# Optimization experiments

Hardware: AMD Instinct MI355X
Metric: run time of the kernel (lower is better)

The kernel has to match this reference:

```python
import jax, jax.numpy as jnp
import numpy as np

D_ATTN = 2048
D_STATE = 64
SHIFT_FRAC = 0.5
LN_EPS = 1e-5


def setup_inputs() -> dict:
    key = jax.random.key(0)
    ks = jax.random.split(key, 8)
    B, T = 8, 2048
    s_attn = 1.0 / np.sqrt(D_ATTN)
    s_state = 1.0 / np.sqrt(D_STATE)
    x = jax.random.normal(ks[0], (B, T, D_ATTN), jnp.float32)
    W_key = jax.random.normal(ks[1], (D_STATE, D_ATTN), jnp.float32) * s_attn
    W_value = jax.random.normal(ks[2], (D_STATE, D_ATTN), jnp.float32) * s_attn
    W_output = jax.random.normal(ks[3], (D_ATTN, D_STATE), jnp.float32) * s_state
    W_shift = jax.random.normal(ks[4], (D_ATTN, D_ATTN), jnp.float32) * s_attn
    gate = jnp.ones((D_ATTN,), jnp.float32)
    # negative decay log so w = exp(time_decay) in (e^-1, 1): stable over T=2048 steps
    time_decay = -jax.random.uniform(ks[5], (D_STATE,), jnp.float32, 0.05, 1.0)
    time_first = jax.random.normal(ks[6], (D_STATE,), jnp.float32) * 0.1
    ln_gamma = jnp.ones((D_ATTN,), jnp.float32)
    ln_beta = jnp.zeros((D_ATTN,), jnp.float32)
    return dict(x=x, W_key=W_key, W_value=W_value, W_output=W_output,
                W_shift=W_shift, gate=gate, time_decay=time_decay,
                time_first=time_first, ln_gamma=ln_gamma, ln_beta=ln_beta)


def reference(x, W_key, W_value, W_output, W_shift, gate, time_decay,
              time_first, ln_gamma, ln_beta):
    B, T, D = x.shape
    # token shift: cat([x[:, s:], x[:, :-s]], dim=1) == roll(x, -s, axis=1)
    shift_len = max(1, int(T * SHIFT_FRAC))
    x_cat = jnp.roll(x, -shift_len, axis=1)
    g = jax.nn.sigmoid(gate)
    x_shift = jnp.einsum('btd,ed->bte', x_cat, W_shift) * g + x * (1.0 - g)
    # LayerNorm over last dim
    mu = jnp.mean(x_shift, axis=-1, keepdims=True)
    var = jnp.var(x_shift, axis=-1, keepdims=True)
    x_norm = (x_shift - mu) * jax.lax.rsqrt(var + LN_EPS) * ln_gamma + ln_beta
    k = jnp.einsum('btd,sd->bts', x_norm, W_key)    # (B,T,Ds)
    v = jnp.einsum('btd,sd->bts', x_norm, W_value)  # (B,T,Ds)
    w = jnp.exp(time_decay)                          # (Ds,)
    u = jnp.exp(time_first)                          # (Ds,)
    wkv = jnp.exp(-u * jax.nn.sigmoid(k)) * v        # (B,T,Ds)
    # linear recurrence: state_t = w * state_{t-1} + wkv_t
    def step(state, wkv_t):
        state = state * w + wkv_t
        return state, state
    init = jnp.zeros((B, k.shape[-1]), x.dtype)
    last_state, states = jax.lax.scan(step, init, jnp.swapaxes(wkv, 0, 1))
    states = jnp.swapaxes(states, 0, 1)              # (B,T,Ds)
    # per-step output projection == single batched GEMM over stacked states
    output = jnp.einsum('bts,ds->btd', states, W_output)  # (B,T,D)
    # dropout in eval mode is identity; last_state is detached in original
    return output, jax.lax.stop_gradient(last_state)
```

## Files before the change

### kernel.cpp

```cpp
#include <hip/hip_runtime.h>
#include <stdint.h>

constexpr int kD  = 2048;
constexpr int kDS = 64;
constexpr int kNT = 2048;
constexpr int kM  = 8 * kNT;
constexpr int kOutElems = kM * kD;

typedef __attribute__((ext_vector_type(8))) short short8;
typedef __attribute__((ext_vector_type(8))) unsigned short bfu8;
typedef __attribute__((ext_vector_type(4))) float f32x4;

__device__ __forceinline__ unsigned short f2bf(float f) {
  unsigned int u = __float_as_uint(f);
  return (unsigned short)((u + 0x7FFFu + ((u >> 16) & 1u)) >> 16);
}
__device__ __forceinline__ float bf2f(unsigned short b) {
  return __uint_as_float(((unsigned int)b) << 16);
}

__device__ __forceinline__ void gload16(const void* g, void* l) {
  __builtin_amdgcn_global_load_lds((__attribute__((address_space(1))) void*)g,
                                   (__attribute__((address_space(3))) void*)l,
                                   16, 0, 0);
}

__global__ void k_cvt(const float* __restrict__ src, unsigned short* __restrict__ dst, int n8) {
  int i8 = blockIdx.x * 256 + threadIdx.x;
  if (i8 >= n8) return;
  const f32x4* s = (const f32x4*)(src + (size_t)i8 * 8);
  f32x4 v0 = s[0], v1 = s[1];
  bfu8 o;
  o[0] = f2bf(v0[0]); o[1] = f2bf(v0[1]); o[2] = f2bf(v0[2]); o[3] = f2bf(v0[3]);
  o[4] = f2bf(v1[0]); o[5] = f2bf(v1[1]); o[6] = f2bf(v1[2]); o[7] = f2bf(v1[3]);
  *(bfu8*)(dst + (size_t)i8 * 8) = o;
}

__global__ void k_cvt_kv(const float* __restrict__ wk, const float* __restrict__ wv,
                         unsigned short* __restrict__ dst) {
  int i8 = blockIdx.x * 256 + threadIdx.x;
  int r = i8 >> 8;
  int dcol = (i8 & 255) << 3;
  int s = r >> 1;
  const float* src = (r & 1) ? wv : wk;
  const f32x4* p = (const f32x4*)(src + (size_t)s * kD + dcol);
  f32x4 v0 = p[0], v1 = p[1];
  bfu8 o;
  o[0] = f2bf(v0[0]); o[1] = f2bf(v0[1]); o[2] = f2bf(v0[2]); o[3] = f2bf(v0[3]);
  o[4] = f2bf(v1[0]); o[5] = f2bf(v1[1]); o[6] = f2bf(v1[2]); o[7] = f2bf(v1[3]);
  *(bfu8*)(dst + (size_t)i8 * 8) = o;
}

#define MM(x,y,z) __builtin_amdgcn_mfma_f32_16x16x32_bf16(x,y,z,0,0,0)
#define BAR __builtin_amdgcn_s_barrier()
#define WAITV_(N) asm volatile("s_waitcnt vmcnt(" #N ")" ::: "memory")
#define WAITV(N) WAITV_(N)
#define WAITL asm volatile("s_waitcnt lgkmcnt(0)")
#define NOWV (void)0

#define STAGEA_TO(BUF,H,Q,KT) gload16(aS + (size_t)(((H)*64+(Q)*128)*2048) + (KT), \
                                      smem + (BUF)*32768 + ((H)*64+(Q)*128)*64 + ldsAst)
#define STAGEB_TO(BUF,H,Q,KT) gload16(bS + (size_t)(((H)*32+(Q)*128)*2048) + (KT), \
                                      smem + (BUF)*32768 + 16384 + (H)*2048 + (Q)*8192 + ldsBst)

#define RDA(CUR,H,MF,KS) (*(const short8*)(smem + (CUR)*32768 + ardb + (H)*4096 + (MF)*1024 + colrd##KS))
#define RDB(CUR,H,NF,KS) (*(const short8*)(smem + (CUR)*32768 + 16384 + brdb + (H)*2048 + (NF)*1024 + colrd##KS))

#define RD_A(CUR,H) \
  a[0][0]=RDA(CUR,H,0,0); a[0][1]=RDA(CUR,H,0,1); \
  a[1][0]=RDA(CUR,H,1,0); a[1][1]=RDA(CUR,H,1,1); \
  a[2][0]=RDA(CUR,H,2,0); a[2][1]=RDA(CUR,H,2,1); \
  a[3][0]=RDA(CUR,H,3,0); a[3][1]=RDA(CUR,H,3,1)
#define RD_B(CUR,H,BV) \
  BV[0][0]=RDB(CUR,H,0,0); BV[0][1]=RDB(CUR,H,0,1); \
  BV[1][0]=RDB(CUR,H,1,0); BV[1][1]=RDB(CUR,H,1,1)

#define MF16(MH, B, NB) \
  __builtin_amdgcn_s_setprio(1); \
  acc[(MH)*4+0][(NB)+0] = MM(a[0][0], B[0][0], acc[(MH)*4+0][(NB)+0]); \
  acc[(MH)*4+0][(NB)+1] = MM(a[0][0], B[1][0], acc[(MH)*4+0][(NB)+1]); \
  acc[(MH)*4+1][(NB)+0] = MM(a[1][0], B[0][0], acc[(MH)*4+1][(NB)+0]); \
  acc[(MH)*4+1][(NB)+1] = MM(a[1][0], B[1][0], acc[(MH)*4+1][(NB)+1]); \
  acc[(MH)*4+2][(NB)+0] = MM(a[2][0], B[0][0], acc[(MH)*4+2][(NB)+0]); \
  acc[(MH)*4+2][(NB)+1] = MM(a[2][0], B[1][0], acc[(MH)*4+2][(NB)+1]); \
  acc[(MH)*4+3][(NB)+0] = MM(a[3][0], B[0][0], acc[(MH)*4+3][(NB)+0]); \
  acc[(MH)*4+3][(NB)+1] = MM(a[3][0], B[1][0], acc[(MH)*4+3][(NB)+1]); \
  acc[(MH)*4+0][(NB)+0] = MM(a[0][1], B[0][1], acc[(MH)*4+0][(NB)+0]); \
  acc[(MH)*4+0][(NB)+1] = MM(a[0][1], B[1][1], acc[(MH)*4+0][(NB)+1]); \
  acc[(MH)*4+1][(NB)+0] = MM(a[1][1], B[0][1], acc[(MH)*4+1][(NB)+0]); \
  acc[(MH)*4+1][(NB)+1] = MM(a[1][1], B[1][1], acc[(MH)*4+1][(NB)+1]); \
  acc[(MH)*4+2][(NB)+0] = MM(a[2][1], B[0][1], acc[(MH)*4+2][(NB)+0]); \
  acc[(MH)*4+2][(NB)+1] = MM(a[2][1], B[1][1], acc[(MH)*4+2][(NB)+1]); \
  acc[(MH)*4+3][(NB)+0] = MM(a[3][1], B[0][1], acc[(MH)*4+3][(NB)+0]); \
  acc[(MH)*4+3][(NB)+1] = MM(a[3][1], B[1][1], acc[(MH)*4+3][(NB)+1]); \
  __builtin_amdgcn_s_setprio(0)

#define PH0(CUR, S, KA1, WV) \
  BAR; WAITL; MF16(0, b0, 0); \
  RD_B(CUR,1,b1); \
  if (S) { STAGEA_TO((CUR)^1, 1, 0, KA1); STAGEA_TO((CUR)^1, 1, 1, KA1); } \
  WV

#define PH1(CUR, S, KT2, WV) \
  BAR; WAITL; MF16(0, b1, 2); \
  RD_A(CUR,1); \
  if (S) { STAGEA_TO(CUR, 0, 0, KT2); STAGEA_TO(CUR, 0, 1, KT2); } \
  WV

#define PH2(CUR, S, KT2, WV) \
  BAR; WAITL; MF16(1, b0, 0); \
  if (S) { STAGEB_TO(CUR, 0, 0, KT2); STAGEB_TO(CUR, 0, 1, KT2); } \
  WV

#define PH3(CUR, RDN, S, KT2, WV) \
  BAR; WAITL; MF16(1, b1, 2); \
  if (RDN) { RD_A((CUR)^1,0); RD_B((CUR)^1,0,b0); } \
  if (S) { STAGEB_TO(CUR, 1, 0, KT2); STAGEB_TO(CUR, 1, 1, KT2); } \
  WV

__global__ __launch_bounds__(512, 2)
void k_gemm_shift8(const unsigned short* __restrict__ A,
                   const unsigned short* __restrict__ Bw,
                   const float* __restrict__ gate,
                   unsigned short* __restrict__ out) {
  __shared__ __align__(16) unsigned char smem_raw[131072];
  unsigned short* smem = (unsigned short*)smem_raw;

  const int tid = threadIdx.x;
  const int lane = tid & 63;
  const int w = tid >> 6;
  const int wr = w >> 2, wc = w & 3;
  const int lr = lane & 15, lq = lane >> 4;
  const int bid = blockIdx.x;
  const int nblk = bid & 7, mblk = bid >> 3;
  const int m0 = mblk * 256, n0 = nblk * 256;

  const int r0 = tid >> 3;
  const int colel = ((tid & 7) * 8) ^ (((tid >> 3) & 7) << 3);
  const unsigned short* aS = A + (size_t)((m0 ^ 1024) + r0) * 2048 + colel;
  const unsigned short* bS = Bw + (size_t)(n0 + ((tid >> 8) << 6) + (r0 & 31)) * 2048 + colel;
  const int ldsAst = tid * 8;
  const int ldsBst = ((tid >> 8) << 12) + (tid & 255) * 8;

  const int ardb = (wr * 128 + lr) * 64;
  const int brdb = (wc * 64 + lr) * 64;
  const int colrd0 = (lq * 8) ^ ((lr & 7) << 3);
  const int colrd1 = (32 + lq * 8) ^ ((lr & 7) << 3);

  short8 a[4][2], b0[2][2], b1[2][2];
  f32x4 acc[8][4] = {};

  STAGEA_TO(0,0,0,0); STAGEA_TO(0,0,1,0);
  STAGEB_TO(0,0,0,0); STAGEB_TO(0,0,1,0);
  STAGEB_TO(0,1,0,0); STAGEB_TO(0,1,1,0);
  STAGEA_TO(0,1,0,0); STAGEA_TO(0,1,1,0);
  STAGEA_TO(1,0,0,64); STAGEA_TO(1,0,1,64);
  STAGEB_TO(1,0,0,64); STAGEB_TO(1,0,1,64);
  STAGEB_TO(1,1,0,64); STAGEB_TO(1,1,1,64);
  WAITV(6); BAR;
  RD_A(0,0); RD_B(0,0,b0);

  int ka1 = 64, kt2 = 128;
  for (int j = 0; j < 15; ++j) {
    PH0(0, 1, ka1, WAITV(8)); PH1(0, 1, kt2, WAITV(8));
    PH2(0, 1, kt2, WAITV(8)); PH3(0, 1, 1, kt2, WAITV(8));
    ka1 += 64; kt2 += 64;
    PH0(1, 1, ka1, WAITV(8)); PH1(1, 1, kt2, WAITV(8));
    PH2(1, 1, kt2, WAITV(8)); PH3(1, 1, 1, kt2, WAITV(8));
    ka1 += 64; kt2 += 64;
  }
  PH0(0, 1, 1984, WAITV(8)); PH1(0, 0, 0, NOWV);
  PH2(0, 0, 0, WAITV(4));    PH3(0, 1, 0, 0, WAITV(2));
  PH0(1, 0, 0, WAITV(0));    PH1(1, 0, 0, NOWV);
  PH2(1, 0, 0, NOWV);        PH3(1, 0, 0, 0, NOWV);

  float* cbuf = (float*)smem_raw;
#pragma unroll
  for (int q = 0; q < 4; ++q) {
    __syncthreads();
    if (wr == (q >> 1)) {
#pragma unroll
      for (int mm = 0; mm < 4; ++mm) {
#pragma unroll
        for (int nf = 0; nf < 4; ++nf) {
#pragma unroll
          for (int i = 0; i < 4; ++i) {
            int rl = mm * 16 + lq * 4 + i;
            int cl = wc * 64 + nf * 16 + lr;
            cbuf[rl * 260 + cl] = acc[(q & 1) * 4 + mm][nf][i];
          }
        }
      }
    }
    __syncthreads();
#pragma unroll
    for (int it = 0; it < 4; ++it) {
      int idx = tid + it * 512;
      int rl = idx >> 5, cb = (idx & 31) * 8;
      int gr = m0 + q * 64 + rl, gc = n0 + cb;
      f32x4 c0 = *(const f32x4*)&cbuf[rl * 260 + cb];
      f32x4 c1 = *(const f32x4*)&cbuf[rl * 260 + cb + 4];
      f32x4 g0 = *(const f32x4*)&gate[gc];
      f32x4 g1 = *(const f32x4*)&gate[gc + 4];
      bfu8 xv = *(const bfu8*)(A + (size_t)gr * 2048 + gc);
      bfu8 o;
#pragma unroll
      for (int jj = 0; jj < 4; ++jj) {
        float g = 1.f / (1.f + __expf(-g0[jj]));
        o[jj] = f2bf(c0[jj] * g + bf2f(xv[jj]) * (1.f - g));
        float h = 1.f / (1.f + __expf(-g1[jj]));
        o[jj + 4] = f2bf(c1[jj] * h + bf2f(xv[jj + 4]) * (1.f - h));
      }
      *(bfu8*)(out + (size_t)gr * 2048 + gc) = o;
    }
  }
}

__launch_bounds__(256)
__global__ void k_ln(const unsigned short* __restrict__ xs, const float* __restrict__ gamma,
                     const float* __restrict__ beta, unsigned short* __restrict__ xn) {
  int m = blockIdx.x;
  int tid = threadIdx.x;
  bfu8 v = *(const bfu8*)(xs + (size_t)m * kD + tid * 8);
  float f[8];
#pragma unroll
  for (int j = 0; j < 8; ++j) f[j] = bf2f(v[j]);
  float s = 0.f, q = 0.f;
#pragma unroll
  for (int j = 0; j < 8; ++j) { s += f[j]; q += f[j] * f[j]; }
#pragma unroll
  for (int d = 1; d < 64; d <<= 1) { s += __shfl_xor(s, d); q += __shfl_xor(q, d); }
  __shared__ float ss[4], qq[4];
  if ((tid & 63) == 0) { ss[tid >> 6] = s; qq[tid >> 6] = q; }
  __syncthreads();
  s = ss[0] + ss[1] + ss[2] + ss[3];
  q = qq[0] + qq[1] + qq[2] + qq[3];
  float mean = s * (1.f / kD);
  float var = q * (1.f / kD) - mean * mean;
  float rstd = rsqrtf(var + 1e-5f);
  int d0 = tid * 8;
  bfu8 o;
#pragma unroll
  for (int j = 0; j < 8; ++j) {
    float g = gamma[d0 + j], b = beta[d0 + j];
    o[j] = f2bf((f[j] - mean) * rstd * g + b);
  }
  *(bfu8*)(xn + (size_t)m * kD + d0) = o;
}

__launch_bounds__(256, 2)
__global__ void k_gemm_kv(const unsigned short* __restrict__ A,
                          const unsigned short* __restrict__ Bw,
                          const float* __restrict__ tfirst,
                          float* __restrict__ wkv) {
  __shared__ __align__(16) unsigned short As[32 * 32];
  __shared__ __align__(16) unsigned short Bs[128 * 32];
  const int tid = threadIdx.x;
  const int lane = tid & 63;
  const int wcv = tid >> 6;
  const int m0 = blockIdx.x * 32;
  const int lr = lane & 15, lk = (lane >> 4) << 3;
  const int c1 = tid, c2 = tid + 256;

  const unsigned short* ga = A + (size_t)(m0 + (tid >> 2)) * kD + ((tid & 3) << 3);
  const unsigned short* gb0 = Bw + (size_t)(c1 >> 2) * kD + ((c1 & 3) << 3);
  const unsigned short* gb1 = Bw + (size_t)(c2 >> 2) * kD + ((c2 & 3) << 3);
  unsigned short* la = As + tid * 8;
  unsigned short* lb0 = Bs + c1 * 8;
  unsigned short* lb1 = Bs + c2 * 8;

  f32x4 acc[2][2] = {};

  for (int kt = 0; kt < kD; kt += 32) {
    __syncthreads();
    if (tid < 128) gload16(ga + kt, la);
    gload16(gb0 + kt, lb0);
    gload16(gb1 + kt, lb1);
    __syncthreads();
    short8 af[2], bf[2];
#pragma unroll
    for (int mf = 0; mf < 2; ++mf)
      af[mf] = *(const short8*)&As[(mf * 16 + lr) * 32 + lk];
#pragma unroll
    for (int nf = 0; nf < 2; ++nf)
      bf[nf] = *(const short8*)&Bs[(wcv * 32 + nf * 16 + lr) * 32 + lk];
#pragma unroll
    for (int mf = 0; mf < 2; ++mf)
#pragma unroll
      for (int nf = 0; nf < 2; ++nf)
        acc[mf][nf] = __builtin_amdgcn_mfma_f32_16x16x32_bf16(af[mf], bf[nf], acc[mf][nf], 0, 0, 0);
  }

  const int fq = lane >> 4, fr = lane & 15;
#pragma unroll
  for (int mf = 0; mf < 2; ++mf) {
#pragma unroll
    for (int nf = 0; nf < 2; ++nf) {
      int c = wcv * 32 + nf * 16 + fr;
#pragma unroll
      for (int i = 0; i < 4; ++i) {
        int r = m0 + mf * 16 + fq * 4 + i;
        float val = acc[mf][nf][i];
        float other = __shfl_xor(val, 1);
        if (!(c & 1)) {
          int s = c >> 1;
          float sk = 1.f / (1.f + expf(-val));
          float u = expf(tfirst[s]);
          wkv[(size_t)r * kDS + s] = expf(-u * sk) * other;
        }
      }
    }
  }
}

__global__ void k_scan(const float* __restrict__ wkv, const float* __restrict__ tdec,
                       unsigned short* __restrict__ states, float* __restrict__ last_state) {
  int chunk = blockIdx.x;
  int b = blockIdx.y;
  int s = threadIdx.x;
  float w = expf(tdec[s]);
  int t1 = chunk * 64;
  int warm = t1 < 256 ? t1 : 256;
  const float* base = wkv + (size_t)b * kNT * kDS + s;
  unsigned short* sbase = states + (size_t)b * kNT * kDS + s;
  float st = 0.f;
#pragma unroll 4
  for (int t = t1 - warm; t < t1; ++t) st = fmaf(st, w, base[(size_t)t * kDS]);
#pragma unroll 4
  for (int t = t1; t < t1 + 64; ++t) {
    st = fmaf(st, w, base[(size_t)t * kDS]);
    sbase[(size_t)t * kDS] = f2bf(st);
  }
  if (chunk == 31) last_state[b * kDS + s] = st;
}

__launch_bounds__(256, 3)
__global__ void k_out_gemm(const unsigned short* __restrict__ states,
                           const unsigned short* __restrict__ Wo,
                           float* __restrict__ out) {
  __shared__ __align__(16) unsigned char sraw[33792];
  unsigned short* As = (unsigned short*)sraw;
  unsigned short* Bs = As + 8192;
  float* cbuf = (float*)sraw;
  const int tid = threadIdx.x;
  const int lane = tid & 63;
  const int w = tid >> 6;
  const int wr = w >> 1, wc = w & 1;
  const int lr = lane & 15, lq = lane >> 4;
  const int n0 = blockIdx.x * 128;
  const int m0 = blockIdx.y * 128;

  const int sr0 = tid >> 3;
  const int scol = ((tid & 7) * 8) ^ (((tid >> 3) & 7) << 3);
#pragma unroll
  for (int rd = 0; rd < 4; ++rd) {
    gload16(states + (size_t)(m0 + sr0 + rd * 32) * 64 + scol, As + tid * 8 + rd * 2048);
    gload16(Wo + (size_t)(n0 + sr0 + rd * 32) * 64 + scol, Bs + tid * 8 + rd * 2048);
  }
  __syncthreads();

  short8 a[4][2], b[4][2];
#pragma unroll
  for (int mf = 0; mf < 4; ++mf) {
#pragma unroll
    for (int ks = 0; ks < 2; ++ks) {
      int col = (ks * 32 + lq * 8) ^ ((lr & 7) << 3);
      a[mf][ks] = *(const short8*)&As[(wr * 64 + mf * 16 + lr) * 64 + col];
      b[mf][ks] = *(const short8*)&Bs[(wc * 64 + mf * 16 + lr) * 64 + col];
    }
  }
  f32x4 acc[4][4] = {};
#pragma unroll
  for (int mf = 0; mf < 4; ++mf)
#pragma unroll
    for (int nf = 0; nf < 4; ++nf) {
      acc[mf][nf] = __builtin_amdgcn_mfma_f32_16x16x32_bf16(a[mf][0], b[nf][0], acc[mf][nf], 0, 0, 0);
      acc[mf][nf] = __builtin_amdgcn_mfma_f32_16x16x32_bf16(a[mf][1], b[nf][1], acc[mf][nf], 0, 0, 0);
    }

#pragma unroll
  for (int q = 0; q < 2; ++q) {
    __syncthreads();
    if (wr == q) {
#pragma unroll
      for (int mf = 0; mf < 4; ++mf)
#pragma unroll
        for (int nf = 0; nf < 4; ++nf)
#pragma unroll
          for (int i = 0; i < 4; ++i) {
            int rl = mf * 16 + lq * 4 + i;
            int cl = wc * 64 + nf * 16 + lr;
            cbuf[rl * 132 + cl] = acc[mf][nf][i];
          }
    }
    __syncthreads();
#pragma unroll
    for (int it = 0; it < 8; ++it) {
      int idx = tid + it * 256;
      int rl = idx >> 5, cb = (idx & 31) * 4;
      *(f32x4*)&out[(size_t)(m0 + q * 64 + rl) * kD + n0 + cb] = *(const f32x4*)&cbuf[rl * 132 + cb];
    }
  }
}

extern "C" void kernel_launch(void* const* d_in, const int* in_sizes, int n_in,
                              void* d_out, int out_size, void* d_ws, size_t ws_size,
                              hipStream_t stream) {
  const float* x    = (const float*)d_in[0];
  const float* Wk   = (const float*)d_in[1];
  const float* Wv   = (const float*)d_in[2];
  const float* Wo   = (const float*)d_in[3];
  const float* Wsh  = (const float*)d_in[4];
  const float* gate = (const float*)d_in[5];
  const float* tdec = (const float*)d_in[6];
  const float* tfir = (const float*)d_in[7];
  const float* lng  = (const float*)d_in[8];
  const float* lnb  = (const float*)d_in[9];
  float* out = (float*)d_out;
  char* ws = (char*)d_ws;

  unsigned short* xbf   = (unsigned short*)(ws);
  unsigned short* wshbf = (unsigned short*)(ws + 67108864);
  unsigned short* wkvbf = (unsigned short*)(ws + 75497472);
  float* wkvf           = (float*)(ws + 76021760);
  unsigned short* stbf  = (unsigned short*)(ws + 80216064);
  unsigned short* wobf  = (unsigned short*)(ws + 82313216);

  k_cvt<<<16384, 256, 0, stream>>>(x, xbf, 4194304);
  k_cvt<<<2048, 256, 0, stream>>>(Wsh, wshbf, 524288);
  k_cvt<<<64, 256, 0, stream>>>(Wo, wobf, 16384);
  k_cvt_kv<<<128, 256, 0, stream>>>(Wk, Wv, wkvbf);

  k_gemm_shift8<<<512, 512, 0, stream>>>(xbf, wshbf, gate, (unsigned short*)out);
  k_ln<<<16384, 256, 0, stream>>>((const unsigned short*)out, lng, lnb, xbf);
  k_gemm_kv<<<512, 256, 0, stream>>>(xbf, wkvbf, tfir, wkvf);
  k_scan<<<dim3(32, 8), 64, 0, stream>>>(wkvf, tdec, stbf, out + kOutElems);
  k_out_gemm<<<dim3(16, 128), 256, 0, stream>>>(stbf, wobf, out);
}
```

Baseline: 289.1 us.

## Fold LayerNorm affine into K/V weights and apply row stats in GEMM epilogue

Replaces the LayerNorm kernel that wrote a normalized bf16 activation with a stats-only kernel that emits per-row mean and rstd. Gamma is folded into the bf16 K/V weights, and per-column sums of gamma*W and beta*W are precomputed. The K/V GEMM now reads the un-normalized shift output directly and applies mean/rstd correction in its epilogue. This removes a full write of the 64MB-class normalized tensor, but the correction k = rstd*(acc - mean*sum) can lose precision through cancellation in bf16-accumulated products.

```diff
diff --git a/kernel.cpp b/kernel.cpp
--- a/kernel.cpp
+++ b/kernel.cpp
@@ -36,19 +36,36 @@
   *(bfu8*)(dst + (size_t)i8 * 8) = o;
 }
 
-__global__ void k_cvt_kv(const float* __restrict__ wk, const float* __restrict__ wv,
-                         unsigned short* __restrict__ dst) {
-  int i8 = blockIdx.x * 256 + threadIdx.x;
-  int r = i8 >> 8;
-  int dcol = (i8 & 255) << 3;
-  int s = r >> 1;
-  const float* src = (r & 1) ? wv : wk;
-  const f32x4* p = (const f32x4*)(src + (size_t)s * kD + dcol);
+__launch_bounds__(256)
+__global__ void k_cvt_kv_g(const float* __restrict__ wk, const float* __restrict__ wv,
+                           const float* __restrict__ gamma, const float* __restrict__ beta,
+                           unsigned short* __restrict__ dst, float2* __restrict__ cgb) {
+  int b = blockIdx.x;
+  int tid = threadIdx.x;
+  int s = b >> 1;
+  const float* src = (b & 1) ? wv : wk;
+  int d0 = tid * 8;
+  const f32x4* p = (const f32x4*)(src + (size_t)s * kD + d0);
   f32x4 v0 = p[0], v1 = p[1];
+  f32x4 g0 = *(const f32x4*)&gamma[d0], g1 = *(const f32x4*)&gamma[d0 + 4];
+  f32x4 b0 = *(const f32x4*)&beta[d0],  b1 = *(const f32x4*)&beta[d0 + 4];
   bfu8 o;
-  o[0] = f2bf(v0[0]); o[1] = f2bf(v0[1]); o[2] = f2bf(v0[2]); o[3] = f2bf(v0[3]);
-  o[4] = f2bf(v1[0]); o[5] = f2bf(v1[1]); o[6] = f2bf(v1[2]); o[7] = f2bf(v1[3]);
-  *(bfu8*)(dst + (size_t)i8 * 8) = o;
+  float sg = 0.f, sb = 0.f;
+#pragma unroll
+  for (int j = 0; j < 4; ++j) {
+    float gw0 = g0[j] * v0[j], gw1 = g1[j] * v1[j];
+    o[j] = f2bf(gw0); o[j + 4] = f2bf(gw1);
+    sg += gw0 + gw1;
+    sb += b0[j] * v0[j] + b1[j] * v1[j];
+  }
+  *(bfu8*)(dst + (size_t)b * kD + d0) = o;
+#pragma unroll
+  for (int d = 1; d < 64; d <<= 1) { sg += __shfl_xor(sg, d); sb += __shfl_xor(sb, d); }
+  __shared__ float gg[4], bb[4];
+  if ((tid & 63) == 0) { gg[tid >> 6] = sg; bb[tid >> 6] = sb; }
+  __syncthreads();
+  if (tid == 0)
+    cgb[b] = make_float2(gg[0] + gg[1] + gg[2] + gg[3], bb[0] + bb[1] + bb[2] + bb[3]);
 }
 
 #define MM(x,y,z) __builtin_amdgcn_mfma_f32_16x16x32_bf16(x,y,z,0,0,0)
@@ -217,44 +234,37 @@
 }
 
 __launch_bounds__(256)
-__global__ void k_ln(const unsigned short* __restrict__ xs, const float* __restrict__ gamma,
-                     const float* __restrict__ beta, unsigned short* __restrict__ xn) {
+__global__ void k_stats(const unsigned short* __restrict__ xs, float2* __restrict__ stats) {
   int m = blockIdx.x;
   int tid = threadIdx.x;
   bfu8 v = *(const bfu8*)(xs + (size_t)m * kD + tid * 8);
-  float f[8];
-#pragma unroll
-  for (int j = 0; j < 8; ++j) f[j] = bf2f(v[j]);
   float s = 0.f, q = 0.f;
 #pragma unroll
-  for (int j = 0; j < 8; ++j) { s += f[j]; q += f[j] * f[j]; }
+  for (int j = 0; j < 8; ++j) { float f = bf2f(v[j]); s += f; q += f * f; }
 #pragma unroll
   for (int d = 1; d < 64; d <<= 1) { s += __shfl_xor(s, d); q += __shfl_xor(q, d); }
   __shared__ float ss[4], qq[4];
   if ((tid & 63) == 0) { ss[tid >> 6] = s; qq[tid >> 6] = q; }
   __syncthreads();
-  s = ss[0] + ss[1] + ss[2] + ss[3];
-  q = qq[0] + qq[1] + qq[2] + qq[3];
-  float mean = s * (1.f / kD);
-  float var = q * (1.f / kD) - mean * mean;
-  float rstd = rsqrtf(var + 1e-5f);
-  int d0 = tid * 8;
-  bfu8 o;
-#pragma unroll
-  for (int j = 0; j < 8; ++j) {
-    float g = gamma[d0 + j], b = beta[d0 + j];
-    o[j] = f2bf((f[j] - mean) * rstd * g + b);
-  }
-  *(bfu8*)(xn + (size_t)m * kD + d0) = o;
+  if (tid == 0) {
+    s = ss[0] + ss[1] + ss[2] + ss[3];
+    q = qq[0] + qq[1] + qq[2] + qq[3];
+    float mean = s * (1.f / kD);
+    float var = q * (1.f / kD) - mean * mean;
+    stats[m] = make_float2(mean, rsqrtf(var + 1e-5f));
+  }
 }
 
 __launch_bounds__(256, 2)
-__global__ void k_gemm_kv(const unsigned short* __restrict__ A,
-                          const unsigned short* __restrict__ Bw,
-                          const float* __restrict__ tfirst,
-                          float* __restrict__ wkv) {
+__global__ void k_gemm_kv_f(const unsigned short* __restrict__ A,
+                            const unsigned short* __restrict__ Bw,
+                            const float2* __restrict__ stats,
+                            const float2* __restrict__ cgb,
+                            const float* __restrict__ tfirst,
+                            float* __restrict__ wkv) {
   __shared__ __align__(16) unsigned short As[32 * 32];
   __shared__ __align__(16) unsigned short Bs[128 * 32];
+  __shared__ float2 rowst[32];
   const int tid = threadIdx.x;
   const int lane = tid & 63;
   const int wcv = tid >> 6;
@@ -262,6 +272,8 @@
   const int lr = lane & 15, lk = (lane >> 4) << 3;
   const int c1 = tid, c2 = tid + 256;
 
+  if (tid < 32) rowst[tid] = stats[m0 + tid];
+
   const unsigned short* ga = A + (size_t)(m0 + (tid >> 2)) * kD + ((tid & 3) << 3);
   const unsigned short* gb0 = Bw + (size_t)(c1 >> 2) * kD + ((c1 & 3) << 3);
   const unsigned short* gb1 = Bw + (size_t)(c2 >> 2) * kD + ((c2 & 3) << 3);
@@ -297,16 +309,18 @@
 #pragma unroll
     for (int nf = 0; nf < 2; ++nf) {
       int c = wcv * 32 + nf * 16 + fr;
+      float2 gc = cgb[c];
 #pragma unroll
       for (int i = 0; i < 4; ++i) {
-        int r = m0 + mf * 16 + fq * 4 + i;
-        float val = acc[mf][nf][i];
+        int rloc = mf * 16 + fq * 4 + i;
+        float2 st = rowst[rloc];
+        float val = st.y * (acc[mf][nf][i] - st.x * gc.x) + gc.y;
         float other = __shfl_xor(val, 1);
         if (!(c & 1)) {
           int s = c >> 1;
           float sk = 1.f / (1.f + expf(-val));
           float u = expf(tfirst[s]);
-          wkv[(size_t)r * kDS + s] = expf(-u * sk) * other;
+          wkv[(size_t)(m0 + rloc) * kDS + s] = expf(-u * sk) * other;
         }
       }
     }
@@ -425,15 +439,17 @@
   float* wkvf           = (float*)(ws + 76021760);
   unsigned short* stbf  = (unsigned short*)(ws + 80216064);
   unsigned short* wobf  = (unsigned short*)(ws + 82313216);
+  float2* statsp        = (float2*)(ws + 82575360);
+  float2* cgbp          = (float2*)(ws + 82706432);
 
   k_cvt<<<16384, 256, 0, stream>>>(x, xbf, 4194304);
   k_cvt<<<2048, 256, 0, stream>>>(Wsh, wshbf, 524288);
   k_cvt<<<64, 256, 0, stream>>>(Wo, wobf, 16384);
-  k_cvt_kv<<<128, 256, 0, stream>>>(Wk, Wv, wkvbf);
+  k_cvt_kv_g<<<128, 256, 0, stream>>>(Wk, Wv, lng, lnb, wkvbf, cgbp);
 
   k_gemm_shift8<<<512, 512, 0, stream>>>(xbf, wshbf, gate, (unsigned short*)out);
-  k_ln<<<16384, 256, 0, stream>>>((const unsigned short*)out, lng, lnb, xbf);
-  k_gemm_kv<<<512, 256, 0, stream>>>(xbf, wkvbf, tfir, wkvf);
+  k_stats<<<16384, 256, 0, stream>>>((const unsigned short*)out, statsp);
+  k_gemm_kv_f<<<512, 256, 0, stream>>>((const unsigned short*)out, wkvbf, statsp, cgbp, tfir, wkvf);
   k_scan<<<dim3(32, 8), 64, 0, stream>>>(wkvf, tdec, stbf, out + kOutElems);
   k_out_gemm<<<dim3(16, 128), 256, 0, stream>>>(stbf, wobf, out);
 }
```

Measured after the change: 275.5 us. -4.7%, faster.
